# Kernel tuning notes

Hardware: AMD Instinct MI355X
Metric: run time of the kernel (lower is better)

The kernel has to match this reference:

```python
import jax, jax.numpy as jnp
import numpy as np

TEMPERATURE = 0.07


def setup_inputs() -> dict:
    key = jax.random.key(0)
    embeddings = jax.random.normal(key, (16384, 256), dtype=jnp.float32)
    return {"embeddings": embeddings}


def reference(embeddings) -> jnp.ndarray:
    # L2 normalize rows (torch F.normalize uses eps clamp 1e-12)
    norm = jnp.maximum(jnp.linalg.norm(embeddings, axis=1, keepdims=True), 1e-12)
    emb = embeddings / norm
    # [N, N] similarity, temperature-scaled logits
    logits = jnp.matmul(emb, emb.T) / TEMPERATURE
    # cross entropy against diagonal labels (labels[i] = i)
    logp = jax.nn.log_softmax(logits, axis=1)
    loss = -jnp.mean(jnp.diagonal(logp))
    return loss
```

## Files before the change

kernel.cpp:

```cpp
#include <hip/hip_runtime.h>
#include <hip/hip_bf16.h>

typedef __bf16 bf16;
typedef __attribute__((ext_vector_type(8))) __bf16 bf16x8;
typedef __attribute__((ext_vector_type(4))) __bf16 bf16x4;
typedef __attribute__((ext_vector_type(16))) float f32x16;

#define N_ROWS 16384
#define DIM 256
#define NJC 512
#define NBLKS 768
#define TPB 43
#define NTILES 33024
#define SQK1 4.53981608f
#define LN2F 0.69314718056f

#define WS_T_OFF (N_ROWS * DIM * 2)
#define WS_D_OFF (WS_T_OFF + N_ROWS * 4)

#define GLOAD_LDS(g, l)                                        \
    __builtin_amdgcn_global_load_lds(                          \
        (const __attribute__((address_space(1))) void*)(g),    \
        (__attribute__((address_space(3))) void*)(l), 16, 0, 0)

__global__ void __launch_bounds__(256) normalize_kernel(const float* __restrict__ in,
                                                        bf16* __restrict__ out,
                                                        float* __restrict__ Tg,
                                                        float* __restrict__ Dg,
                                                        float* __restrict__ loss_out) {
    if (blockIdx.x == 0 && threadIdx.x == 0) loss_out[0] = 0.0f;
    if (blockIdx.x < 64) Tg[blockIdx.x * 256 + threadIdx.x] = 0.0f;

    const int row  = blockIdx.x * 4 + (threadIdx.x >> 6);
    const int lane = threadIdx.x & 63;
    const float4* rp = (const float4*)(in + (size_t)row * DIM);
    float4 v = rp[lane];
    float ss = v.x * v.x + v.y * v.y + v.z * v.z + v.w * v.w;
#pragma unroll
    for (int m = 1; m < 64; m <<= 1) ss += __shfl_xor(ss, m, 64);
    float inv = SQK1 / fmaxf(sqrtf(ss), 1e-12f);
    bf16x4 o;
    o[0] = (bf16)(v.x * inv);
    o[1] = (bf16)(v.y * inv);
    o[2] = (bf16)(v.z * inv);
    o[3] = (bf16)(v.w * inv);
    *(bf16x4*)(out + (size_t)row * DIM + lane * 4) = o;

    float f0 = (float)o[0], f1 = (float)o[1], f2 = (float)o[2], f3 = (float)o[3];
    float s2 = f0 * f0 + f1 * f1 + f2 * f2 + f3 * f3;
#pragma unroll
    for (int m = 1; m < 64; m <<= 1) s2 += __shfl_xor(s2, m, 64);
    if (lane == 0) Dg[row] = s2;
}

#define TREE16(R, out)                                                     \
    do {                                                                   \
        float w8[8], w4[4], w2[2], w1, g_;                                 \
        _Pragma("unroll") for (int i_ = 0; i_ < 8; ++i_) {                 \
            g_ = (lo & 16) ? R[i_] : R[i_ + 8];                            \
            w8[i_] = ((lo & 16) ? R[i_ + 8] : R[i_]) + __shfl_xor(g_, 16); \
        }                                                                  \
        _Pragma("unroll") for (int i_ = 0; i_ < 4; ++i_) {                 \
            g_ = (lo & 8) ? w8[i_] : w8[i_ + 4];                           \
            w4[i_] = ((lo & 8) ? w8[i_ + 4] : w8[i_]) + __shfl_xor(g_, 8); \
        }                                                                  \
        _Pragma("unroll") for (int i_ = 0; i_ < 2; ++i_) {                 \
            g_ = (lo & 4) ? w4[i_] : w4[i_ + 2];                           \
            w2[i_] = ((lo & 4) ? w4[i_ + 2] : w4[i_]) + __shfl_xor(g_, 4); \
        }                                                                  \
        g_ = (lo & 2) ? w2[0] : w2[1];                                     \
        w1 = ((lo & 2) ? w2[1] : w2[0]) + __shfl_xor(g_, 2);               \
        out = w1 + __shfl_xor(w1, 1);                                      \
    } while (0)

__global__ void __launch_bounds__(256, 3)
loss_kernel(const bf16* __restrict__ A, float* __restrict__ Tg) {
    __shared__ bf16 Bs0[32 * DIM];
    __shared__ bf16 Bs1[32 * DIM];

    const int tid = threadIdx.x;
    const int w  = tid >> 6;
    const int l  = tid & 63;
    const int lo = l & 31, hi = l >> 5;

    const int tbeg = blockIdx.x * TPB;
    const int nrem = TPB;

    int it = 0;
    while (2 * (it + 1) * (257 - (it + 1)) <= tbeg) ++it;
    int jc = 4 * it + (tbeg - 2 * it * (257 - it));

    bf16x8 af[16];
#define LOAD_AF                                                              \
    do {                                                                     \
        const bf16* ap_ = A + (size_t)(it * 128 + w * 32 + lo) * DIM + hi * 8; \
        _Pragma("unroll") for (int k_ = 0; k_ < 16; ++k_)                    \
            af[k_] = *(const bf16x8*)(ap_ + k_ * 16);                        \
    } while (0)
    LOAD_AF;

    float s0[16];
#pragma unroll
    for (int r = 0; r < 16; ++r) s0[r] = 0.f;

    const int s_dma = l & 31;
    const int rl    = l >> 5;
    int vo[4];
#pragma unroll
    for (int q = 0; q < 4; ++q) {
        const int c = (s_dma & 24) | ((s_dma & 7) ^ ((q * 2 + rl) & 7));
        vo[q] = rl * DIM + c * 8;
    }

    const int rbase = lo * DIM;
    const int mx7 = lo & 7;

#define ISSUE(jcn_, BUF)                                                     \
    do {                                                                     \
        const bf16* tb_ = A + (size_t)((jcn_) * 32 + w * 8) * DIM;           \
        bf16* lb_ = &BUF[(w * 8) * DIM];                                     \
        _Pragma("unroll") for (int q_ = 0; q_ < 4; ++q_) {                   \
            GLOAD_LDS(tb_ + (q_ * 2) * DIM + vo[q_],                         \
                      lb_ + (q_ * 2) * DIM);                                 \
        }                                                                    \
    } while (0)

#define FLUSH_ROWS                                                           \
    do {                                                                     \
        float tr_;                                                           \
        TREE16(s0, tr_);                                                     \
        const int r_ = (lo >> 1) & 15;                                       \
        const int rowoff_ = (r_ & 3) + 8 * (r_ >> 2) + 4 * hi;               \
        if ((l & 1) == 0)                                                    \
            atomicAdd(&Tg[it * 128 + w * 32 + rowoff_], tr_);                \
    } while (0)

    int t = 0, jcn, itn;
    bool has_next;

#define NEXT_DECODE                                                          \
    do {                                                                     \
        has_next = (t + 1 < nrem);                                           \
        if (has_next) {                                                      \
            jcn = jc + 1; itn = it;                                          \
            if (jcn == NJC) { itn = it + 1; jcn = 4 * itn; }                 \
        } else { jcn = jc; itn = it; }                                       \
    } while (0)

#define TILE_BODY(BR, BW, WN, WL)                                            \
    do {                                                                     \
        asm volatile("s_barrier" ::: "memory");                              \
        if (has_next) {                                                      \
            ISSUE(jcn, BW);                                                  \
            asm volatile("s_waitcnt vmcnt(" #WN ")" ::: "memory");           \
        } else {                                                             \
            asm volatile("s_waitcnt vmcnt(" #WL ")" ::: "memory");           \
        }                                                                    \
        asm volatile("s_barrier" ::: "memory");                              \
        f32x16 c0;                                                           \
        _Pragma("unroll") for (int r_ = 0; r_ < 16; ++r_) c0[r_] = 0.f;      \
        __builtin_amdgcn_s_setprio(1);                                       \
        _Pragma("unroll") for (int k_ = 0; k_ < 16; ++k_) {                  \
            const int cc_ = k_ * 2 + hi;                                     \
            const int slot_ = (cc_ & 24) | ((cc_ & 7) ^ mx7);                \
            bf16x8 b_ = *(const bf16x8*)&BR[rbase + slot_ * 8];              \
            c0 = __builtin_amdgcn_mfma_f32_32x32x16_bf16(af[k_], b_, c0, 0, 0, 0); \
        }                                                                    \
        __builtin_amdgcn_s_setprio(0);                                       \
        float cs_ = 0.f;                                                     \
        _Pragma("unroll") for (int r_ = 0; r_ < 16; ++r_) {                  \
            float e_ = __builtin_amdgcn_exp2f(c0[r_]);                       \
            s0[r_] += e_;                                                    \
            cs_ += e_;                                                       \
        }                                                                    \
        cs_ += __shfl_xor(cs_, 32);                                          \
         \
         \
        const float fv_ = ((jc >> 2) == it) ? 0.0f : cs_;                    \
        if (hi == 0) atomicAdd(&Tg[jc * 32 + lo], fv_);                      \
    } while (0)

#define ADVANCE                                                              \
    do {                                                                     \
        ++t;                                                                 \
        if (itn != it) {                                                     \
            FLUSH_ROWS;                                                      \
            it = itn;                                                        \
            LOAD_AF;                                                         \
            _Pragma("unroll") for (int r_ = 0; r_ < 16; ++r_) s0[r_] = 0.f;  \
        }                                                                    \
        jc = jcn;                                                            \
    } while (0)

    ISSUE(jc, Bs0);
    NEXT_DECODE;
    TILE_BODY(Bs0, Bs1, 4, 0);
    ADVANCE;
    while (t < nrem) {
        NEXT_DECODE;
        TILE_BODY(Bs1, Bs0, 5, 1);
        ADVANCE;
        if (t >= nrem) break;
        NEXT_DECODE;
        TILE_BODY(Bs0, Bs1, 5, 1);
        ADVANCE;
    }
    FLUSH_ROWS;

#undef ISSUE
#undef TILE_BODY
#undef NEXT_DECODE
#undef ADVANCE
#undef FLUSH_ROWS
#undef LOAD_AF
}

__global__ void __launch_bounds__(256) final_kernel(const float* __restrict__ Tg,
                                                    const float* __restrict__ Dg,
                                                    float* __restrict__ out) {
    __shared__ float red[4];
    const int i = blockIdx.x * 256 + threadIdx.x;
    float c = LN2F * (__log2f(Tg[i]) - Dg[i]) * (1.0f / (float)N_ROWS);
#pragma unroll
    for (int m = 1; m < 64; m <<= 1) c += __shfl_xor(c, m, 64);
    if ((threadIdx.x & 63) == 0) red[threadIdx.x >> 6] = c;
    __syncthreads();
    if (threadIdx.x == 0)
        atomicAdd(out, red[0] + red[1] + red[2] + red[3]);
}

extern "C" void kernel_launch(void* const* d_in, const int* in_sizes, int n_in,
                              void* d_out, int out_size, void* d_ws, size_t ws_size,
                              hipStream_t stream) {
    const float* emb = (const float*)d_in[0];
    float* out = (float*)d_out;
    bf16* Abf = (bf16*)d_ws;
    float* Tg = (float*)((char*)d_ws + WS_T_OFF);
    float* Dg = (float*)((char*)d_ws + WS_D_OFF);

    hipLaunchKernelGGL(normalize_kernel, dim3(N_ROWS / 4), dim3(256), 0, stream,
                       emb, Abf, Tg, Dg, out);
    hipLaunchKernelGGL(loss_kernel, dim3(NBLKS), dim3(256), 0, stream,
                       Abf, Tg);
    hipLaunchKernelGGL(final_kernel, dim3(N_ROWS / 256), dim3(256), 0, stream,
                       Tg, Dg, out);
}
```

Measured before the change: 147.3 us.

## Triple-buffer LDS tile prefetch and swizzle block-to-tile mapping

Moves from a double-buffered to a triple-buffered LDS pipeline, so the global-to-LDS load for tile t+2 is issued after a single barrier while tile t is computed. This drops one barrier per tile and gives loads more time in flight. It also remaps blockIdx so consecutive hardware blocks take tiles spread across the triangle, which changes L2 locality and balance across XCDs. LDS use grows from 32KB to 48KB per block, which could limit occupancy at 3 blocks per CU.

Measured after the change: 148.5 us. About the same (+0.8%).

```diff
diff --git a/kernel.cpp b/kernel.cpp
--- a/kernel.cpp
+++ b/kernel.cpp
@@ -75,29 +75,33 @@
 
 __global__ void __launch_bounds__(256, 3)
 loss_kernel(const bf16* __restrict__ A, float* __restrict__ Tg) {
-    __shared__ bf16 Bs0[32 * DIM];
-    __shared__ bf16 Bs1[32 * DIM];
+    __shared__ bf16 Bs[3][32 * DIM];
 
     const int tid = threadIdx.x;
     const int w  = tid >> 6;
     const int l  = tid & 63;
     const int lo = l & 31, hi = l >> 5;
 
-    const int tbeg = blockIdx.x * TPB;
-    const int nrem = TPB;
+    const int bid = (int)(blockIdx.x & 7) * (NBLKS / 8) + (int)(blockIdx.x >> 3);
+    const int tbeg = bid * TPB;
 
     int it = 0;
     while (2 * (it + 1) * (257 - (it + 1)) <= tbeg) ++it;
     int jc = 4 * it + (tbeg - 2 * it * (257 - it));
 
+#define ADV(ITX, JCX)                                                        \
+    do { if (++JCX == NJC) { ++ITX; JCX = 4 * ITX; } } while (0)
+    int it1 = it, jc1 = jc; ADV(it1, jc1);
+    int it2 = it1, jc2 = jc1; ADV(it2, jc2);
+
     bf16x8 af[16];
-#define LOAD_AF                                                              \
-    do {                                                                     \
-        const bf16* ap_ = A + (size_t)(it * 128 + w * 32 + lo) * DIM + hi * 8; \
+#define LOAD_AF(ITX)                                                         \
+    do {                                                                     \
+        const bf16* ap_ = A + (size_t)((ITX) * 128 + w * 32 + lo) * DIM + hi * 8; \
         _Pragma("unroll") for (int k_ = 0; k_ < 16; ++k_)                    \
             af[k_] = *(const bf16x8*)(ap_ + k_ * 16);                        \
     } while (0)
-    LOAD_AF;
+    LOAD_AF(it);
 
     float s0[16];
 #pragma unroll
@@ -118,7 +122,7 @@
 #define ISSUE(jcn_, BUF)                                                     \
     do {                                                                     \
         const bf16* tb_ = A + (size_t)((jcn_) * 32 + w * 8) * DIM;           \
-        bf16* lb_ = &BUF[(w * 8) * DIM];                                     \
+        bf16* lb_ = (BUF) + (w * 8) * DIM;                                   \
         _Pragma("unroll") for (int q_ = 0; q_ < 4; ++q_) {                   \
             GLOAD_LDS(tb_ + (q_ * 2) * DIM + vo[q_],                         \
                       lb_ + (q_ * 2) * DIM);                                 \
@@ -135,35 +139,24 @@
             atomicAdd(&Tg[it * 128 + w * 32 + rowoff_], tr_);                \
     } while (0)
 
-    int t = 0, jcn, itn;
-    bool has_next;
-
-#define NEXT_DECODE                                                          \
-    do {                                                                     \
-        has_next = (t + 1 < nrem);                                           \
-        if (has_next) {                                                      \
-            jcn = jc + 1; itn = it;                                          \
-            if (jcn == NJC) { itn = it + 1; jcn = 4 * itn; }                 \
-        } else { jcn = jc; itn = it; }                                       \
-    } while (0)
-
-#define TILE_BODY(BR, BW, WN, WL)                                            \
-    do {                                                                     \
-        asm volatile("s_barrier" ::: "memory");                              \
-        if (has_next) {                                                      \
-            ISSUE(jcn, BW);                                                  \
-            asm volatile("s_waitcnt vmcnt(" #WN ")" ::: "memory");           \
+    int t = 0;
+
+#define BODY(BR, BW, WN0, WL)                                                \
+    do {                                                                     \
+        if (t + 2 < TPB) {                                                   \
+            asm volatile("s_waitcnt vmcnt(" #WN0 ")" ::: "memory");          \
         } else {                                                             \
             asm volatile("s_waitcnt vmcnt(" #WL ")" ::: "memory");           \
         }                                                                    \
         asm volatile("s_barrier" ::: "memory");                              \
+        if (t + 2 < TPB) ISSUE(jc2, BW);                                     \
         f32x16 c0;                                                           \
         _Pragma("unroll") for (int r_ = 0; r_ < 16; ++r_) c0[r_] = 0.f;      \
         __builtin_amdgcn_s_setprio(1);                                       \
         _Pragma("unroll") for (int k_ = 0; k_ < 16; ++k_) {                  \
             const int cc_ = k_ * 2 + hi;                                     \
             const int slot_ = (cc_ & 24) | ((cc_ & 7) ^ mx7);                \
-            bf16x8 b_ = *(const bf16x8*)&BR[rbase + slot_ * 8];              \
+            bf16x8 b_ = *(const bf16x8*)&(BR)[rbase + slot_ * 8];            \
             c0 = __builtin_amdgcn_mfma_f32_32x32x16_bf16(af[k_], b_, c0, 0, 0, 0); \
         }                                                                    \
         __builtin_amdgcn_s_setprio(0);                                       \
@@ -178,39 +171,33 @@
          \
         const float fv_ = ((jc >> 2) == it) ? 0.0f : cs_;                    \
         if (hi == 0) atomicAdd(&Tg[jc * 32 + lo], fv_);                      \
-    } while (0)
-
-#define ADVANCE                                                              \
-    do {                                                                     \
+        if (t + 1 < TPB) {                                                   \
+            if (it1 != it) {                                                 \
+                FLUSH_ROWS;                                                  \
+                LOAD_AF(it1);                                                \
+                _Pragma("unroll") for (int r_ = 0; r_ < 16; ++r_) s0[r_] = 0.f; \
+            }                                                                \
+            it = it1; jc = jc1; it1 = it2; jc1 = jc2; ADV(it2, jc2);         \
+        }                                                                    \
         ++t;                                                                 \
-        if (itn != it) {                                                     \
-            FLUSH_ROWS;                                                      \
-            it = itn;                                                        \
-            LOAD_AF;                                                         \
-            _Pragma("unroll") for (int r_ = 0; r_ < 16; ++r_) s0[r_] = 0.f;  \
-        }                                                                    \
-        jc = jcn;                                                            \
-    } while (0)
-
-    ISSUE(jc, Bs0);
-    NEXT_DECODE;
-    TILE_BODY(Bs0, Bs1, 4, 0);
-    ADVANCE;
-    while (t < nrem) {
-        NEXT_DECODE;
-        TILE_BODY(Bs1, Bs0, 5, 1);
-        ADVANCE;
-        if (t >= nrem) break;
-        NEXT_DECODE;
-        TILE_BODY(Bs0, Bs1, 5, 1);
-        ADVANCE;
+    } while (0)
+
+    ISSUE(jc, &Bs[0][0]);
+    ISSUE(jc1, &Bs[1][0]);
+
+    BODY(&Bs[0][0], &Bs[2][0], 4, 0);
+    while (t < TPB) {
+        BODY(&Bs[1][0], &Bs[0][0], 5, 1);
+        if (t >= TPB) break;
+        BODY(&Bs[2][0], &Bs[1][0], 5, 1);
+        if (t >= TPB) break;
+        BODY(&Bs[0][0], &Bs[2][0], 5, 1);
     }
     FLUSH_ROWS;
 
 #undef ISSUE
-#undef TILE_BODY
-#undef NEXT_DECODE
-#undef ADVANCE
+#undef BODY
+#undef ADV
 #undef FLUSH_ROWS
 #undef LOAD_AF
 }
```

## Fuse normalize, loss and final reduction into one cooperative grid-synced kernel

Applied to the files above, without the earlier changes.

Replaces the three separate kernel launches with a single cooperative kernel. It normalizes rows in a grid-stride loop, does a grid.sync, runs the same tiled MFMA log-sum-exp loop, syncs again, and has block 0 compute the final loss. The aim is to remove launch gaps and inter-kernel drain between stages. The cost is two grid-wide barriers, a serial final reduction done by one block, and an occupancy query on the host each call, with a fallback to the old three-kernel path if the cooperative launch fails.

After: 287.1 us. 94.9% more time.

```diff
diff --git a/kernel.cpp b/kernel.cpp
--- a/kernel.cpp
+++ b/kernel.cpp
@@ -1,5 +1,8 @@
 #include <hip/hip_runtime.h>
 #include <hip/hip_bf16.h>
+#include <hip/hip_cooperative_groups.h>
+
+namespace cg = cooperative_groups;
 
 typedef __bf16 bf16;
 typedef __attribute__((ext_vector_type(8))) __bf16 bf16x8;
@@ -12,6 +15,7 @@
 #define NBLKS 768
 #define TPB 43
 #define NTILES 33024
+#define NCU 256
 #define SQK1 4.53981608f
 #define LN2F 0.69314718056f
 
@@ -22,36 +26,6 @@
     __builtin_amdgcn_global_load_lds(                          \
         (const __attribute__((address_space(1))) void*)(g),    \
         (__attribute__((address_space(3))) void*)(l), 16, 0, 0)
-
-__global__ void __launch_bounds__(256) normalize_kernel(const float* __restrict__ in,
-                                                        bf16* __restrict__ out,
-                                                        float* __restrict__ Tg,
-                                                        float* __restrict__ Dg,
-                                                        float* __restrict__ loss_out) {
-    if (blockIdx.x == 0 && threadIdx.x == 0) loss_out[0] = 0.0f;
-    if (blockIdx.x < 64) Tg[blockIdx.x * 256 + threadIdx.x] = 0.0f;
-
-    const int row  = blockIdx.x * 4 + (threadIdx.x >> 6);
-    const int lane = threadIdx.x & 63;
-    const float4* rp = (const float4*)(in + (size_t)row * DIM);
-    float4 v = rp[lane];
-    float ss = v.x * v.x + v.y * v.y + v.z * v.z + v.w * v.w;
-#pragma unroll
-    for (int m = 1; m < 64; m <<= 1) ss += __shfl_xor(ss, m, 64);
-    float inv = SQK1 / fmaxf(sqrtf(ss), 1e-12f);
-    bf16x4 o;
-    o[0] = (bf16)(v.x * inv);
-    o[1] = (bf16)(v.y * inv);
-    o[2] = (bf16)(v.z * inv);
-    o[3] = (bf16)(v.w * inv);
-    *(bf16x4*)(out + (size_t)row * DIM + lane * 4) = o;
-
-    float f0 = (float)o[0], f1 = (float)o[1], f2 = (float)o[2], f3 = (float)o[3];
-    float s2 = f0 * f0 + f1 * f1 + f2 * f2 + f3 * f3;
-#pragma unroll
-    for (int m = 1; m < 64; m <<= 1) s2 += __shfl_xor(s2, m, 64);
-    if (lane == 0) Dg[row] = s2;
-}
 
 #define TREE16(R, out)                                                     \
     do {                                                                   \
@@ -73,6 +47,37 @@
         out = w1 + __shfl_xor(w1, 1);                                      \
     } while (0)
 
+
+__global__ void __launch_bounds__(256) normalize_kernel(const float* __restrict__ in,
+                                                        bf16* __restrict__ out,
+                                                        float* __restrict__ Tg,
+                                                        float* __restrict__ Dg,
+                                                        float* __restrict__ loss_out) {
+    if (blockIdx.x == 0 && threadIdx.x == 0) loss_out[0] = 0.0f;
+    if (blockIdx.x < 64) Tg[blockIdx.x * 256 + threadIdx.x] = 0.0f;
+
+    const int row  = blockIdx.x * 4 + (threadIdx.x >> 6);
+    const int lane = threadIdx.x & 63;
+    const float4* rp = (const float4*)(in + (size_t)row * DIM);
+    float4 v = rp[lane];
+    float ss = v.x * v.x + v.y * v.y + v.z * v.z + v.w * v.w;
+#pragma unroll
+    for (int m = 1; m < 64; m <<= 1) ss += __shfl_xor(ss, m, 64);
+    float inv = SQK1 / fmaxf(sqrtf(ss), 1e-12f);
+    bf16x4 o;
+    o[0] = (bf16)(v.x * inv);
+    o[1] = (bf16)(v.y * inv);
+    o[2] = (bf16)(v.z * inv);
+    o[3] = (bf16)(v.w * inv);
+    *(bf16x4*)(out + (size_t)row * DIM + lane * 4) = o;
+
+    float f0 = (float)o[0], f1 = (float)o[1], f2 = (float)o[2], f3 = (float)o[3];
+    float s2 = f0 * f0 + f1 * f1 + f2 * f2 + f3 * f3;
+#pragma unroll
+    for (int m = 1; m < 64; m <<= 1) s2 += __shfl_xor(s2, m, 64);
+    if (lane == 0) Dg[row] = s2;
+}
+
 __global__ void __launch_bounds__(256, 3)
 loss_kernel(const bf16* __restrict__ A, float* __restrict__ Tg) {
     __shared__ bf16 Bs0[32 * DIM];
@@ -174,8 +179,6 @@
             cs_ += e_;                                                       \
         }                                                                    \
         cs_ += __shfl_xor(cs_, 32);                                          \
-         \
-         \
         const float fv_ = ((jc >> 2) == it) ? 0.0f : cs_;                    \
         if (hi == 0) atomicAdd(&Tg[jc * 32 + lo], fv_);                      \
     } while (0)
@@ -229,6 +232,213 @@
         atomicAdd(out, red[0] + red[1] + red[2] + red[3]);
 }
 
+__global__ void __launch_bounds__(256, 3)
+fused_kernel(const float* __restrict__ in, bf16* __restrict__ A,
+             float* __restrict__ Tg, float* __restrict__ Dg,
+             float* __restrict__ out, int nblks) {
+    __shared__ bf16 Bs0[32 * DIM];
+    __shared__ bf16 Bs1[32 * DIM];
+    __shared__ float red[4];
+
+    cg::grid_group grid = cg::this_grid();
+
+    const int tid = threadIdx.x;
+    const int bid = (int)blockIdx.x;
+
+    {
+        if (bid < 64)
+            __hip_atomic_store(&Tg[bid * 256 + tid], 0.0f,
+                               __ATOMIC_RELAXED, __HIP_MEMORY_SCOPE_AGENT);
+        const int lane = tid & 63;
+        for (int rg = bid; rg < (N_ROWS / 4); rg += nblks) {
+            const int row = rg * 4 + (tid >> 6);
+            const float4* rp = (const float4*)(in + (size_t)row * DIM);
+            float4 v = rp[lane];
+            float ss = v.x * v.x + v.y * v.y + v.z * v.z + v.w * v.w;
+#pragma unroll
+            for (int m = 1; m < 64; m <<= 1) ss += __shfl_xor(ss, m, 64);
+            float inv = SQK1 / fmaxf(sqrtf(ss), 1e-12f);
+            bf16x4 o;
+            o[0] = (bf16)(v.x * inv);
+            o[1] = (bf16)(v.y * inv);
+            o[2] = (bf16)(v.z * inv);
+            o[3] = (bf16)(v.w * inv);
+            union { bf16x4 v4; unsigned long long u64; } pun;
+            pun.v4 = o;
+            __hip_atomic_store(
+                reinterpret_cast<unsigned long long*>(A + (size_t)row * DIM + lane * 4),
+                pun.u64, __ATOMIC_RELAXED, __HIP_MEMORY_SCOPE_AGENT);
+
+            float f0 = (float)o[0], f1 = (float)o[1];
+            float f2 = (float)o[2], f3 = (float)o[3];
+            float s2 = f0 * f0 + f1 * f1 + f2 * f2 + f3 * f3;
+#pragma unroll
+            for (int m = 1; m < 64; m <<= 1) s2 += __shfl_xor(s2, m, 64);
+            if (lane == 0)
+                __hip_atomic_store(&Dg[row], s2,
+                                   __ATOMIC_RELAXED, __HIP_MEMORY_SCOPE_AGENT);
+        }
+    }
+
+    grid.sync();
+
+    {
+        const int w  = tid >> 6;
+        const int l  = tid & 63;
+        const int lo = l & 31, hi = l >> 5;
+
+        const int tbeg = (int)(((long long)bid * NTILES) / nblks);
+        const int tend = (int)(((long long)(bid + 1) * NTILES) / nblks);
+        const int nrem = tend - tbeg;
+
+        int it = 0;
+        while (2 * (it + 1) * (257 - (it + 1)) <= tbeg) ++it;
+        int jc = 4 * it + (tbeg - 2 * it * (257 - it));
+
+        bf16x8 af[16];
+#define LOAD_AF                                                              \
+    do {                                                                     \
+        const bf16* ap_ = A + (size_t)(it * 128 + w * 32 + lo) * DIM + hi * 8; \
+        _Pragma("unroll") for (int k_ = 0; k_ < 16; ++k_)                    \
+            af[k_] = *(const bf16x8*)(ap_ + k_ * 16);                        \
+    } while (0)
+        LOAD_AF;
+
+        float s0[16];
+#pragma unroll
+        for (int r = 0; r < 16; ++r) s0[r] = 0.f;
+
+        const int s_dma = l & 31;
+        const int rl    = l >> 5;
+        int vo[4];
+#pragma unroll
+        for (int q = 0; q < 4; ++q) {
+            const int c = (s_dma & 24) | ((s_dma & 7) ^ ((q * 2 + rl) & 7));
+            vo[q] = rl * DIM + c * 8;
+        }
+
+        const int rbase = lo * DIM;
+        const int mx7 = lo & 7;
+
+#define ISSUE(jcn_, BUF)                                                     \
+    do {                                                                     \
+        const bf16* tb_ = A + (size_t)((jcn_) * 32 + w * 8) * DIM;           \
+        bf16* lb_ = &BUF[(w * 8) * DIM];                                     \
+        _Pragma("unroll") for (int q_ = 0; q_ < 4; ++q_) {                   \
+            GLOAD_LDS(tb_ + (q_ * 2) * DIM + vo[q_],                         \
+                      lb_ + (q_ * 2) * DIM);                                 \
+        }                                                                    \
+    } while (0)
+
+#define FLUSH_ROWS                                                           \
+    do {                                                                     \
+        float tr_;                                                           \
+        TREE16(s0, tr_);                                                     \
+        const int r_ = (lo >> 1) & 15;                                       \
+        const int rowoff_ = (r_ & 3) + 8 * (r_ >> 2) + 4 * hi;               \
+        if ((l & 1) == 0)                                                    \
+            atomicAdd(&Tg[it * 128 + w * 32 + rowoff_], tr_);                \
+    } while (0)
+
+        int t = 0, jcn, itn;
+        bool has_next;
+
+#define NEXT_DECODE                                                          \
+    do {                                                                     \
+        has_next = (t + 1 < nrem);                                           \
+        if (has_next) {                                                      \
+            jcn = jc + 1; itn = it;                                          \
+            if (jcn == NJC) { itn = it + 1; jcn = 4 * itn; }                 \
+        } else { jcn = jc; itn = it; }                                       \
+    } while (0)
+
+#define TILE_BODY(BR, BW, WN, WL)                                            \
+    do {                                                                     \
+        asm volatile("s_barrier" ::: "memory");                              \
+        if (has_next) {                                                      \
+            ISSUE(jcn, BW);                                                  \
+            asm volatile("s_waitcnt vmcnt(" #WN ")" ::: "memory");           \
+        } else {                                                             \
+            asm volatile("s_waitcnt vmcnt(" #WL ")" ::: "memory");           \
+        }                                                                    \
+        asm volatile("s_barrier" ::: "memory");                              \
+        f32x16 c0;                                                           \
+        _Pragma("unroll") for (int r_ = 0; r_ < 16; ++r_) c0[r_] = 0.f;      \
+        __builtin_amdgcn_s_setprio(1);                                       \
+        _Pragma("unroll") for (int k_ = 0; k_ < 16; ++k_) {                  \
+            const int cc_ = k_ * 2 + hi;                                     \
+            const int slot_ = (cc_ & 24) | ((cc_ & 7) ^ mx7);                \
+            bf16x8 b_ = *(const bf16x8*)&BR[rbase + slot_ * 8];              \
+            c0 = __builtin_amdgcn_mfma_f32_32x32x16_bf16(af[k_], b_, c0, 0, 0, 0); \
+        }                                                                    \
+        __builtin_amdgcn_s_setprio(0);                                       \
+        float cs_ = 0.f;                                                     \
+        _Pragma("unroll") for (int r_ = 0; r_ < 16; ++r_) {                  \
+            float e_ = __builtin_amdgcn_exp2f(c0[r_]);                       \
+            s0[r_] += e_;                                                    \
+            cs_ += e_;                                                       \
+        }                                                                    \
+        cs_ += __shfl_xor(cs_, 32);                                          \
+        const float fv_ = ((jc >> 2) == it) ? 0.0f : cs_;                    \
+        if (hi == 0) atomicAdd(&Tg[jc * 32 + lo], fv_);                      \
+    } while (0)
+
+#define ADVANCE                                                              \
+    do {                                                                     \
+        ++t;                                                                 \
+        if (itn != it) {                                                     \
+            FLUSH_ROWS;                                                      \
+            it = itn;                                                        \
+            LOAD_AF;                                                         \
+            _Pragma("unroll") for (int r_ = 0; r_ < 16; ++r_) s0[r_] = 0.f;  \
+        }                                                                    \
+        jc = jcn;                                                            \
+    } while (0)
+
+        ISSUE(jc, Bs0);
+        NEXT_DECODE;
+        TILE_BODY(Bs0, Bs1, 4, 0);
+        ADVANCE;
+        while (t < nrem) {
+            NEXT_DECODE;
+            TILE_BODY(Bs1, Bs0, 5, 1);
+            ADVANCE;
+            if (t >= nrem) break;
+            NEXT_DECODE;
+            TILE_BODY(Bs0, Bs1, 5, 1);
+            ADVANCE;
+        }
+        FLUSH_ROWS;
+
+#undef ISSUE
+#undef TILE_BODY
+#undef NEXT_DECODE
+#undef ADVANCE
+#undef FLUSH_ROWS
+#undef LOAD_AF
+    }
+
+    grid.sync();
+
+    if (bid == 0) {
+        float c = 0.f;
+        for (int i = tid; i < N_ROWS; i += 256) {
+            float tv = __hip_atomic_load(&Tg[i], __ATOMIC_RELAXED,
+                                         __HIP_MEMORY_SCOPE_AGENT);
+            float dv = __hip_atomic_load(&Dg[i], __ATOMIC_RELAXED,
+                                         __HIP_MEMORY_SCOPE_AGENT);
+            c += __log2f(tv) - dv;
+        }
+#pragma unroll
+        for (int m = 1; m < 64; m <<= 1) c += __shfl_xor(c, m, 64);
+        if ((tid & 63) == 0) red[tid >> 6] = c;
+        __syncthreads();
+        if (tid == 0)
+            out[0] = LN2F * (red[0] + red[1] + red[2] + red[3])
+                     * (1.0f / (float)N_ROWS);
+    }
+}
+
 extern "C" void kernel_launch(void* const* d_in, const int* in_sizes, int n_in,
                               void* d_out, int out_size, void* d_ws, size_t ws_size,
                               hipStream_t stream) {
@@ -238,10 +448,24 @@
     float* Tg = (float*)((char*)d_ws + WS_T_OFF);
     float* Dg = (float*)((char*)d_ws + WS_D_OFF);
 
-    hipLaunchKernelGGL(normalize_kernel, dim3(N_ROWS / 4), dim3(256), 0, stream,
-                       emb, Abf, Tg, Dg, out);
-    hipLaunchKernelGGL(loss_kernel, dim3(NBLKS), dim3(256), 0, stream,
-                       Abf, Tg);
-    hipLaunchKernelGGL(final_kernel, dim3(N_ROWS / 256), dim3(256), 0, stream,
-                       Tg, Dg, out);
+    int maxPerCU = 0;
+    hipError_t qe = hipOccupancyMaxActiveBlocksPerMultiprocessor(
+        &maxPerCU, fused_kernel, 256, 0);
+    int nblks = NBLKS;
+    if (qe == hipSuccess && maxPerCU >= 1 && maxPerCU * NCU < nblks)
+        nblks = maxPerCU * NCU;
+    if (nblks < 64) nblks = 64;
+
+    void* args[] = {(void*)&emb, (void*)&Abf, (void*)&Tg, (void*)&Dg,
+                    (void*)&out, (void*)&nblks};
+    hipError_t le = hipLaunchCooperativeKernel(fused_kernel, dim3(nblks),
+                                               dim3(256), args, 0, stream);
+    if (le != hipSuccess) {
+        hipLaunchKernelGGL(normalize_kernel, dim3(N_ROWS / 4), dim3(256), 0,
+                           stream, emb, Abf, Tg, Dg, out);
+        hipLaunchKernelGGL(loss_kernel, dim3(NBLKS), dim3(256), 0, stream,
+                           Abf, Tg);
+        hipLaunchKernelGGL(final_kernel, dim3(N_ROWS / 256), dim3(256), 0,
+                           stream, Tg, Dg, out);
+    }
 }
```
